# Kernel tuning notes

Measured on AMD Instinct MI355X. Metric: run time of the kernel, lower is better.

Reference implementation:

```python
import jax, jax.numpy as jnp
import numpy as np

N, E = 8192, 262144
IN_DIM, OUT_DIM = 256, 256


def setup_inputs() -> dict:
    key = jax.random.key(0)
    k = jax.random.split(key, 7)
    x = jax.random.normal(k[0], (N, IN_DIM), dtype=jnp.float32)
    edge_index = jax.random.randint(k[1], (2, E), 0, N, dtype=jnp.int64)
    # parameters (nn.Linear stores weight as (out, in); bias=False everywhere)
    W = jax.random.normal(k[2], (OUT_DIM, IN_DIM), dtype=jnp.float32) / np.sqrt(IN_DIM)
    a_src = jax.random.normal(k[3], (OUT_DIM,), dtype=jnp.float32) / np.sqrt(OUT_DIM)
    a_dst = jax.random.normal(k[4], (OUT_DIM,), dtype=jnp.float32) / np.sqrt(OUT_DIM)
    gamma = jnp.ones((OUT_DIM,), dtype=jnp.float32)
    beta = jnp.zeros((OUT_DIM,), dtype=jnp.float32)
    return {"x": x, "edge_index": edge_index, "W": W, "a_src": a_src,
            "a_dst": a_dst, "gamma": gamma, "beta": beta}


def reference(x, edge_index, W, a_src, a_dst, gamma, beta):
    h = x @ W.T                                     # (N, D)
    src, dst = edge_index[0], edge_index[1]
    s_src = h @ a_src                               # (N,) attn_src logits
    s_dst = h @ a_dst                               # (N,)
    e = jax.nn.leaky_relu(s_src[src] + s_dst[dst], negative_slope=0.2)  # (E,)
    n = x.shape[0]
    # dense scatter: attn[dst, src] = e (duplicate edges overwrite, like torch)
    attn = jnp.zeros((n, n), dtype=x.dtype).at[dst, src].set(e)
    attn = jax.nn.softmax(attn + (attn == 0).astype(x.dtype) * -1e9, axis=-1)
    attn = attn * (attn > 1e-6).astype(x.dtype)
    out = attn @ h                                  # (N, D)
    z = jax.nn.elu(out) + h
    # LayerNorm (eps=1e-5, biased variance, matching torch)
    mean = jnp.mean(z, axis=-1, keepdims=True)
    var = jnp.var(z, axis=-1, keepdims=True)
    return gamma * (z - mean) * jax.lax.rsqrt(var + 1e-5) + beta
```

## Files before the change

kernel.cpp:

```cpp
#include <hip/hip_runtime.h>
#include <math.h>

#define N_NODES 8192
#define EDGES   262144
#define D       256
#define ROWCAP  128
#define PITCH   68


__global__ __launch_bounds__(256)
void gemm_h(const float* __restrict__ x, const float* __restrict__ W,
            const float* __restrict__ a_src, const float* __restrict__ a_dst,
            float* __restrict__ h, float* __restrict__ s_src,
            float* __restrict__ s_dst) {
  __shared__ float As[32][PITCH];
  __shared__ float Bs[32][PITCH];
  const int bm = blockIdx.x * 64;
  const int bj = blockIdx.y * 64;
  const int tid = threadIdx.x;
  const int tr = tid >> 4, tc = tid & 15;
  float acc[4][4] = {{0.f}};
  for (int k0 = 0; k0 < D; k0 += 32) {
#pragma unroll
    for (int f = 0; f < 2; ++f) {
      int idx = tid + f * 256;
      int r = idx >> 3, c4 = (idx & 7) << 2;
      float4 va = *reinterpret_cast<const float4*>(&x[(size_t)(bm + r) * D + k0 + c4]);
      As[c4][r] = va.x; As[c4 + 1][r] = va.y; As[c4 + 2][r] = va.z; As[c4 + 3][r] = va.w;
      float4 vb = *reinterpret_cast<const float4*>(&W[(size_t)(bj + r) * D + k0 + c4]);
      Bs[c4][r] = vb.x; Bs[c4 + 1][r] = vb.y; Bs[c4 + 2][r] = vb.z; Bs[c4 + 3][r] = vb.w;
    }
    __syncthreads();
#pragma unroll
    for (int k = 0; k < 32; ++k) {
      float4 a4 = *reinterpret_cast<const float4*>(&As[k][tr * 4]);
      float4 b4 = *reinterpret_cast<const float4*>(&Bs[k][tc * 4]);
      float a[4] = {a4.x, a4.y, a4.z, a4.w};
      float b[4] = {b4.x, b4.y, b4.z, b4.w};
#pragma unroll
      for (int i = 0; i < 4; ++i)
#pragma unroll
        for (int j = 0; j < 4; ++j)
          acc[i][j] = fmaf(a[i], b[j], acc[i][j]);
    }
    __syncthreads();
  }
  float4 asv = *reinterpret_cast<const float4*>(&a_src[bj + tc * 4]);
  float4 adv = *reinterpret_cast<const float4*>(&a_dst[bj + tc * 4]);
#pragma unroll
  for (int i = 0; i < 4; ++i) {
    float4 v = make_float4(acc[i][0], acc[i][1], acc[i][2], acc[i][3]);
    *reinterpret_cast<float4*>(&h[(size_t)(bm + tr * 4 + i) * D + bj + tc * 4]) = v;
    float ps = v.x * asv.x + v.y * asv.y + v.z * asv.z + v.w * asv.w;
    float pd = v.x * adv.x + v.y * adv.y + v.z * adv.z + v.w * adv.w;
#pragma unroll
    for (int off = 8; off; off >>= 1) {
      ps += __shfl_down(ps, off, 16);
      pd += __shfl_down(pd, off, 16);
    }
    if (tc == 0) {
      atomicAdd(&s_src[bm + tr * 4 + i], ps);
      atomicAdd(&s_dst[bm + tr * 4 + i], pd);
    }
  }
}

__global__ __launch_bounds__(256)
void scatter_kernel(const int* __restrict__ ei, int* __restrict__ fill,
                    int* __restrict__ csr) {
  int lane = threadIdx.x & 63;
  unsigned long long b = __ballot(ei[lane * 2 + 1] == 0);
  int is64 = (b == 0xFFFFFFFFFFFFFFFFull) ? 1 : 0;
  int e = blockIdx.x * 256 + threadIdx.x;
  int src, dst;
  if (is64) { src = ei[2 * e];  dst = ei[2 * (EDGES + e)]; }
  else      { src = ei[e];      dst = ei[EDGES + e]; }
  int p = atomicAdd(&fill[dst], 1);
  if (p < ROWCAP) csr[dst * ROWCAP + p] = src;
}

__global__ __launch_bounds__(256)
void row_fused(const float* __restrict__ h, const float* __restrict__ s_src,
               const float* __restrict__ s_dst, const int* __restrict__ fill,
               const int* __restrict__ csr, const float* __restrict__ gamma,
               const float* __restrict__ beta, float* __restrict__ out) {
  __shared__ int   s_idx[ROWCAP];
  __shared__ float s_w[ROWCAP];
  __shared__ float red[8];
  const int row  = blockIdx.x;
  const int tid  = threadIdx.x;
  const int lane = tid & 63, wid = tid >> 6;
  int len = fill[row];
  if (len > ROWCAP) len = ROWCAP;
  const float sd = s_dst[row];

  for (int i = tid; i < len; i += 256) s_idx[i] = csr[row * ROWCAP + i];
  __syncthreads();

  float lmax = -3.0e38f;
  for (int i = tid; i < len; i += 256) {
    int s = s_idx[i];
    bool dup = false;
    for (int j = 0; j < i; ++j)
      if (s_idx[j] == s) { dup = true; break; }
    float v;
    if (dup) {
      v = -3.0e38f;
    } else {
      v = s_src[s] + sd;
      v = (v >= 0.f) ? v : 0.2f * v;
      if (v == 0.0f) v = -3.0e38f;
    }
    s_w[i] = v;
    lmax = fmaxf(lmax, v);
  }
#pragma unroll
  for (int off = 32; off; off >>= 1) lmax = fmaxf(lmax, __shfl_down(lmax, off, 64));
  if (lane == 0) red[wid] = lmax;
  __syncthreads();
  lmax = fmaxf(fmaxf(red[0], red[1]), fmaxf(red[2], red[3]));

  float lsum = 0.f;
  for (int i = tid; i < len; i += 256) {
    float e = expf(s_w[i] - lmax);
    s_w[i] = e;
    lsum += e;
  }
#pragma unroll
  for (int off = 32; off; off >>= 1) lsum += __shfl_down(lsum, off, 64);
  if (lane == 0) red[4 + wid] = lsum;
  __syncthreads();
  lsum = red[4] + red[5] + red[6] + red[7];
  float inv = 1.0f / lsum;
  for (int i = tid; i < len; i += 256) {
    float w = s_w[i] * inv;
    s_w[i] = (w > 1e-6f) ? w : 0.f;
  }
  __syncthreads();

  float acc = 0.f;
#pragma unroll 4
  for (int i = 0; i < len; ++i)
    acc += s_w[i] * h[(size_t)s_idx[i] * D + tid];

  float z = ((acc > 0.f) ? acc : expm1f(acc)) + h[(size_t)row * D + tid];

  float v1 = z;
#pragma unroll
  for (int off = 32; off; off >>= 1) v1 += __shfl_down(v1, off, 64);
  if (lane == 0) red[wid] = v1;
  __syncthreads();
  float mean = (red[0] + red[1] + red[2] + red[3]) * (1.0f / 256.0f);
  __syncthreads();
  float d = z - mean;
  float v2 = d * d;
#pragma unroll
  for (int off = 32; off; off >>= 1) v2 += __shfl_down(v2, off, 64);
  if (lane == 0) red[wid] = v2;
  __syncthreads();
  float var = (red[0] + red[1] + red[2] + red[3]) * (1.0f / 256.0f);
  out[(size_t)row * D + tid] = gamma[tid] * d * rsqrtf(var + 1e-5f) + beta[tid];
}

extern "C" void kernel_launch(void* const* d_in, const int* in_sizes, int n_in,
                              void* d_out, int out_size, void* d_ws, size_t ws_size,
                              hipStream_t stream) {
  const float* x     = (const float*)d_in[0];
  const int*   ei    = (const int*)d_in[1];
  const float* W     = (const float*)d_in[2];
  const float* a_src = (const float*)d_in[3];
  const float* a_dst = (const float*)d_in[4];
  const float* gamma = (const float*)d_in[5];
  const float* beta  = (const float*)d_in[6];
  float* out = (float*)d_out;

  char* ws = (char*)d_ws;
  int*   fill   = (int*)(ws);
  float* s_src  = (float*)(ws + 32768);
  float* s_dst  = (float*)(ws + 65536);
  int*   csr    = (int*)(ws + 98304);
  float* h      = (float*)(ws + 4292608);
  if (ws_size < 12681216) return;

  hipMemsetAsync(ws, 0, 98304, stream);
  gemm_h<<<dim3(N_NODES / 64, D / 64), 256, 0, stream>>>(x, W, a_src, a_dst,
                                                         h, s_src, s_dst);
  scatter_kernel<<<EDGES / 256, 256, 0, stream>>>(ei, fill, csr);
  row_fused<<<N_NODES, 256, 0, stream>>>(h, s_src, s_dst, fill, csr, gamma, beta, out);
}
```

Before: 152.0 us.

## Process one row per wavefront with float4 gathers in fused row kernel

The row kernel now gives each 64-lane wavefront its own destination row, four rows per block, instead of one row per 256-thread block. Each lane handles four features with float4 gathers of h, unrolled four neighbors at a time. Cross-wave shared-memory reductions and most block barriers become wave-level xor shuffles. This cuts synchronization and turns scalar loads into wider ones, but it leaves less parallelism per row for the serial duplicate-check loop, and rows with a long tail of neighbors can hold back the other waves at the remaining barrier.

```diff
diff --git a/kernel.cpp b/kernel.cpp
--- a/kernel.cpp
+++ b/kernel.cpp
@@ -84,25 +84,25 @@
                const float* __restrict__ s_dst, const int* __restrict__ fill,
                const int* __restrict__ csr, const float* __restrict__ gamma,
                const float* __restrict__ beta, float* __restrict__ out) {
-  __shared__ int   s_idx[ROWCAP];
-  __shared__ float s_w[ROWCAP];
-  __shared__ float red[8];
-  const int row  = blockIdx.x;
-  const int tid  = threadIdx.x;
-  const int lane = tid & 63, wid = tid >> 6;
+  __shared__ int   s_idx[4][ROWCAP];
+  __shared__ float s_w[4][ROWCAP];
+  const int w    = threadIdx.x >> 6;
+  const int lane = threadIdx.x & 63;
+  const int row  = blockIdx.x * 4 + w;
   int len = fill[row];
   if (len > ROWCAP) len = ROWCAP;
+  const int len_pad = (len + 3) & ~3;
   const float sd = s_dst[row];
 
-  for (int i = tid; i < len; i += 256) s_idx[i] = csr[row * ROWCAP + i];
+  for (int i = lane; i < len; i += 64) s_idx[w][i] = csr[row * ROWCAP + i];
   __syncthreads();
 
   float lmax = -3.0e38f;
-  for (int i = tid; i < len; i += 256) {
-    int s = s_idx[i];
+  for (int i = lane; i < len; i += 64) {
+    int s = s_idx[w][i];
     bool dup = false;
     for (int j = 0; j < i; ++j)
-      if (s_idx[j] == s) { dup = true; break; }
+      if (s_idx[w][j] == s) { dup = true; break; }
     float v;
     if (dup) {
       v = -3.0e38f;
@@ -111,55 +111,66 @@
       v = (v >= 0.f) ? v : 0.2f * v;
       if (v == 0.0f) v = -3.0e38f;
     }
-    s_w[i] = v;
+    s_w[w][i] = v;
     lmax = fmaxf(lmax, v);
   }
 #pragma unroll
-  for (int off = 32; off; off >>= 1) lmax = fmaxf(lmax, __shfl_down(lmax, off, 64));
-  if (lane == 0) red[wid] = lmax;
+  for (int off = 32; off; off >>= 1) lmax = fmaxf(lmax, __shfl_xor(lmax, off, 64));
+
+  float lsum = 0.f;
+  for (int i = lane; i < len; i += 64) {
+    float e = expf(s_w[w][i] - lmax);
+    s_w[w][i] = e;
+    lsum += e;
+  }
+#pragma unroll
+  for (int off = 32; off; off >>= 1) lsum += __shfl_xor(lsum, off, 64);
+  float inv = (lsum > 0.f) ? (1.0f / lsum) : 0.f;
+  for (int i = lane; i < len; i += 64) {
+    float ww = s_w[w][i] * inv;
+    s_w[w][i] = (ww > 1e-6f) ? ww : 0.f;
+  }
+  for (int i = len + lane; i < len_pad; i += 64) { s_w[w][i] = 0.f; s_idx[w][i] = 0; }
   __syncthreads();
-  lmax = fmaxf(fmaxf(red[0], red[1]), fmaxf(red[2], red[3]));
-
-  float lsum = 0.f;
-  for (int i = tid; i < len; i += 256) {
-    float e = expf(s_w[i] - lmax);
-    s_w[i] = e;
-    lsum += e;
-  }
-#pragma unroll
-  for (int off = 32; off; off >>= 1) lsum += __shfl_down(lsum, off, 64);
-  if (lane == 0) red[4 + wid] = lsum;
-  __syncthreads();
-  lsum = red[4] + red[5] + red[6] + red[7];
-  float inv = 1.0f / lsum;
-  for (int i = tid; i < len; i += 256) {
-    float w = s_w[i] * inv;
-    s_w[i] = (w > 1e-6f) ? w : 0.f;
-  }
-  __syncthreads();
-
-  float acc = 0.f;
-#pragma unroll 4
-  for (int i = 0; i < len; ++i)
-    acc += s_w[i] * h[(size_t)s_idx[i] * D + tid];
-
-  float z = ((acc > 0.f) ? acc : expm1f(acc)) + h[(size_t)row * D + tid];
-
-  float v1 = z;
-#pragma unroll
-  for (int off = 32; off; off >>= 1) v1 += __shfl_down(v1, off, 64);
-  if (lane == 0) red[wid] = v1;
-  __syncthreads();
-  float mean = (red[0] + red[1] + red[2] + red[3]) * (1.0f / 256.0f);
-  __syncthreads();
-  float d = z - mean;
-  float v2 = d * d;
-#pragma unroll
-  for (int off = 32; off; off >>= 1) v2 += __shfl_down(v2, off, 64);
-  if (lane == 0) red[wid] = v2;
-  __syncthreads();
-  float var = (red[0] + red[1] + red[2] + red[3]) * (1.0f / 256.0f);
-  out[(size_t)row * D + tid] = gamma[tid] * d * rsqrtf(var + 1e-5f) + beta[tid];
+
+  float4 acc = make_float4(0.f, 0.f, 0.f, 0.f);
+  for (int i = 0; i < len_pad; i += 4) {
+    float w0 = s_w[w][i], w1 = s_w[w][i + 1], w2 = s_w[w][i + 2], w3 = s_w[w][i + 3];
+    const float4 h0 = *reinterpret_cast<const float4*>(&h[(size_t)s_idx[w][i]     * D + lane * 4]);
+    const float4 h1 = *reinterpret_cast<const float4*>(&h[(size_t)s_idx[w][i + 1] * D + lane * 4]);
+    const float4 h2 = *reinterpret_cast<const float4*>(&h[(size_t)s_idx[w][i + 2] * D + lane * 4]);
+    const float4 h3 = *reinterpret_cast<const float4*>(&h[(size_t)s_idx[w][i + 3] * D + lane * 4]);
+    acc.x = fmaf(w0, h0.x, fmaf(w1, h1.x, fmaf(w2, h2.x, fmaf(w3, h3.x, acc.x))));
+    acc.y = fmaf(w0, h0.y, fmaf(w1, h1.y, fmaf(w2, h2.y, fmaf(w3, h3.y, acc.y))));
+    acc.z = fmaf(w0, h0.z, fmaf(w1, h1.z, fmaf(w2, h2.z, fmaf(w3, h3.z, acc.z))));
+    acc.w = fmaf(w0, h0.w, fmaf(w1, h1.w, fmaf(w2, h2.w, fmaf(w3, h3.w, acc.w))));
+  }
+
+  const float4 hr = *reinterpret_cast<const float4*>(&h[(size_t)row * D + lane * 4]);
+  float4 z;
+  z.x = ((acc.x > 0.f) ? acc.x : expm1f(acc.x)) + hr.x;
+  z.y = ((acc.y > 0.f) ? acc.y : expm1f(acc.y)) + hr.y;
+  z.z = ((acc.z > 0.f) ? acc.z : expm1f(acc.z)) + hr.z;
+  z.w = ((acc.w > 0.f) ? acc.w : expm1f(acc.w)) + hr.w;
+
+  float s1 = z.x + z.y + z.z + z.w;
+#pragma unroll
+  for (int off = 32; off; off >>= 1) s1 += __shfl_xor(s1, off, 64);
+  float mean = s1 * (1.0f / 256.0f);
+  float dx = z.x - mean, dy = z.y - mean, dz = z.z - mean, dw = z.w - mean;
+  float s2 = dx * dx + dy * dy + dz * dz + dw * dw;
+#pragma unroll
+  for (int off = 32; off; off >>= 1) s2 += __shfl_xor(s2, off, 64);
+  float rs = rsqrtf(s2 * (1.0f / 256.0f) + 1e-5f);
+
+  const float4 gm = *reinterpret_cast<const float4*>(&gamma[lane * 4]);
+  const float4 bt = *reinterpret_cast<const float4*>(&beta[lane * 4]);
+  float4 o;
+  o.x = gm.x * dx * rs + bt.x;
+  o.y = gm.y * dy * rs + bt.y;
+  o.z = gm.z * dz * rs + bt.z;
+  o.w = gm.w * dw * rs + bt.w;
+  *reinterpret_cast<float4*>(&out[(size_t)row * D + lane * 4]) = o;
 }
 
 extern "C" void kernel_launch(void* const* d_in, const int* in_sizes, int n_in,
@@ -186,5 +197,5 @@
   gemm_h<<<dim3(N_NODES / 64, D / 64), 256, 0, stream>>>(x, W, a_src, a_dst,
                                                          h, s_src, s_dst);
   scatter_kernel<<<EDGES / 256, 256, 0, stream>>>(ei, fill, csr);
-  row_fused<<<N_NODES, 256, 0, stream>>>(h, s_src, s_dst, fill, csr, gamma, beta, out);
-}
+  row_fused<<<N_NODES / 4, 256, 0, stream>>>(h, s_src, s_dst, fill, csr, gamma, beta, out);
+}
```

New measurement: 137.9 us. -9.2%, faster.
